# Optimization experiments

Measured on AMD Instinct MI355X. Metric: run time of the kernel, lower is better.

Reference implementation:

```python
import jax, jax.numpy as jnp
import numpy as np

N_NODES = 50000
N_EDGES = 800000
N_GRAPHS = 256
W_SCALE = 0.05  # keep activations bounded through 5 relu conv layers


def setup_inputs() -> dict:
    key = jax.random.key(0)
    ks = jax.random.split(key, 16)
    rn = lambda k, shape: W_SCALE * jax.random.normal(k, shape, dtype=jnp.float32)
    return {
        "x": jax.random.normal(ks[0], (N_NODES, 336), dtype=jnp.float32),
        "edge_index": jax.random.randint(ks[1], (2, N_EDGES), 0, N_NODES, dtype=jnp.int32),
        "batch": jnp.sort(jax.random.randint(ks[2], (N_NODES,), 0, N_GRAPHS, dtype=jnp.int32)),
        "w1_rel": rn(ks[3], (100, 336)),
        "w1_root": rn(ks[4], (100, 336)),
        "b1": rn(ks[5], (100,)),
        "w_rel": rn(ks[6], (4, 100, 100)),
        "w_root": rn(ks[7], (4, 100, 100)),
        "b": rn(ks[8], (4, 100)),
        "lw1": rn(ks[9], (100, 100)),
        "lb1": rn(ks[10], (100,)),
        "lw2": rn(ks[11], (100, 100)),
        "lb2": rn(ks[12], (100,)),
        "lw3": rn(ks[13], (29, 100)),
        "lb3": rn(ks[14], (29,)),
    }


def _graph_conv(x, edge_index, w_rel, w_root, bias):
    # PyG GraphConv: out_i = W_rel @ (sum_{j->i} x_j) + b + W_root @ x_i
    src, dst = edge_index[0], edge_index[1]
    agg = jax.ops.segment_sum(x[src], dst, num_segments=x.shape[0])  # [N, d_in]
    return agg @ w_rel.T + bias + x @ w_root.T


def reference(x, edge_index, batch, w1_rel, w1_root, b1, w_rel, w_root, b,
              lw1, lb1, lw2, lb2, lw3, lb3):
    h = jax.nn.relu(_graph_conv(x, edge_index, w1_rel, w1_root, b1))  # [N,100]
    for i in range(4):  # conv2..conv5 (structurally distinct params)
        h = jax.nn.relu(_graph_conv(h, edge_index, w_rel[i], w_root[i], b[i]))
    # global_mean_pool over graphs
    sums = jax.ops.segment_sum(h, batch, num_segments=N_GRAPHS)          # [G,100]
    counts = jax.ops.segment_sum(jnp.ones((h.shape[0],), h.dtype), batch,
                                 num_segments=N_GRAPHS)                  # [G]
    pooled = sums / jnp.maximum(counts, 1.0)[:, None]
    h = jax.nn.relu(pooled @ lw1.T + lb1)
    h = jax.nn.relu(h @ lw2.T + lb2)
    return h @ lw3.T + lb3  # [G, 29]
```

## Files before the change

### kernel.cpp

```cpp
#include <hip/hip_runtime.h>

#define N_NODES 50000
#define N_EDGES 800000
#define N_GRAPHS 256
#define F 100

#define SCAN_B 512
#define SCAN_NB 98
#define SCAN_PAD (SCAN_NB * SCAN_B)

#define PART_SZ 6250
#define FILL_CHUNK 2048

#define SROW 72
#define EPS 264
#define AST 264

typedef __attribute__((ext_vector_type(8))) short bf16x8;
typedef __attribute__((ext_vector_type(4))) float f32x4;
typedef unsigned short ushort_t;
typedef unsigned int uint_t;

__device__ inline ushort_t f2bf(float f) {
  uint_t u = __float_as_uint(f);
  uint_t r = (u + 0x7fffu + ((u >> 16) & 1u)) >> 16;
  return (ushort_t)r;
}


__global__ __launch_bounds__(256) void hist_kernel(const int* __restrict__ dst,
                                                   int* __restrict__ cnt, int E) {
  int part = blockIdx.x & 7;
  int lo = part * PART_SZ, hi = lo + PART_SZ;
  int base = (blockIdx.x >> 3) * FILL_CHUNK;
  int end = base + FILL_CHUNK; if (end > E) end = E;
  for (int i = base + threadIdx.x; i < end; i += 256) {
    int d = dst[i];
    if (d >= lo && d < hi) atomicAdd(&cnt[d], 1);
  }
}

__global__ __launch_bounds__(SCAN_B) void scan1_kernel(const int* __restrict__ cnt,
                                                       int* __restrict__ excl,
                                                       int* __restrict__ bsum) {
  __shared__ int sh[SCAN_B];
  int t = threadIdx.x;
  int i = blockIdx.x * SCAN_B + t;
  int v = cnt[i];
  sh[t] = v;
  __syncthreads();
  for (int off = 1; off < SCAN_B; off <<= 1) {
    int u = (t >= off) ? sh[t - off] : 0;
    __syncthreads();
    sh[t] += u;
    __syncthreads();
  }
  excl[i] = sh[t] - v;
  if (t == SCAN_B - 1) bsum[blockIdx.x] = sh[t];
}

__global__ __launch_bounds__(128) void scan2_kernel(int* __restrict__ bsum) {
  __shared__ int sh[128];
  int t = threadIdx.x;
  int v = (t < SCAN_NB) ? bsum[t] : 0;
  sh[t] = v;
  __syncthreads();
  for (int off = 1; off < 128; off <<= 1) {
    int u = (t >= off) ? sh[t - off] : 0;
    __syncthreads();
    sh[t] += u;
    __syncthreads();
  }
  if (t < SCAN_NB) bsum[t] = sh[t] - v;
}

__global__ __launch_bounds__(SCAN_B) void scan3_kernel(const int* __restrict__ excl,
                                                       const int* __restrict__ bsum,
                                                       int* __restrict__ offs,
                                                       int* __restrict__ cursor) {
  int i = blockIdx.x * SCAN_B + threadIdx.x;
  int v = excl[i] + bsum[blockIdx.x];
  if (i <= N_NODES) { offs[i] = v; cursor[i] = v; }
}

__global__ __launch_bounds__(256) void fill_kernel(const int* __restrict__ src,
                                                   const int* __restrict__ dst,
                                                   int* __restrict__ cursor,
                                                   int* __restrict__ csr_src, int E) {
  int part = blockIdx.x & 7;
  int lo = part * PART_SZ, hi = lo + PART_SZ;
  int base = (blockIdx.x >> 3) * FILL_CHUNK;
  int end = base + FILL_CHUNK; if (end > E) end = E;
  for (int i = base + threadIdx.x; i < end; i += 256) {
    int d = dst[i];
    if (d >= lo && d < hi) {
      int p = atomicAdd(&cursor[d], 1);
      csr_src[p] = src[i];
    }
  }
}


__global__ void pack_w1_kernel(const float* __restrict__ w1_rel, const float* __restrict__ w1_root,
                               ushort_t* __restrict__ Wp1) {
  int row = blockIdx.x;
  for (int k = threadIdx.x; k < 384; k += 128) {
    float v = 0.f;
    if (k < 336) {
      if (row < 100) v = w1_rel[row * 336 + k];
      else if (row < 200) v = w1_root[(row - 100) * 336 + k];
    }
    Wp1[(size_t)row * 384 + k] = f2bf(v);
  }
}

__global__ void pack_wf_kernel(const float* __restrict__ w_rel, const float* __restrict__ w_root,
                               ushort_t* __restrict__ Wf) {
  int rowl = blockIdx.x;
  int l = rowl >> 7, row = rowl & 127;
  int k = threadIdx.x;
  float v = 0.f;
  if (row < 100) {
    if (k < 100) v = w_rel[((size_t)l * 100 + row) * 100 + k];
    else if (k >= 128 && k < 228) v = w_root[((size_t)l * 100 + row) * 100 + (k - 128)];
  }
  Wf[(size_t)rowl * 256 + k] = f2bf(v);
}


template <bool AF32>
__global__ __launch_bounds__(256) void conv_mfma(
    const void* __restrict__ Aptr, const ushort_t* __restrict__ Wp,
    const float* __restrict__ bias,
    ushort_t* __restrict__ ZP, int Kp) {
  __shared__ short smem[64 * SROW + 208 * SROW];
  __shared__ float bias_s[104];
  short* alds = smem;
  short* blds = smem + 64 * SROW;

  int tid = threadIdx.x;
  int n0 = blockIdx.x * 64;
  if (tid < 100) bias_s[tid] = bias[tid];

  f32x4 acc[13];
#pragma unroll
  for (int b = 0; b < 13; ++b) acc[b] = (f32x4)0.f;

  int w = tid >> 6, lane = tid & 63, q = lane >> 4, m16 = lane & 15;

  int ar[2], aq[2];
#pragma unroll
  for (int u = 0; u < 2; ++u) { int c = tid + u * 256; ar[u] = c >> 3; aq[u] = c & 7; }

  bf16x8 areg[2], breg[7];

  auto load_chunk = [&](int k0) {
#pragma unroll
    for (int u = 0; u < 2; ++u) {
      int node = n0 + ar[u];
      int k = k0 + aq[u] * 8;
      bf16x8 val = (bf16x8)0;
      if (AF32) {
        if (node < N_NODES && k < 336) {
          const float* p = (const float*)Aptr + (size_t)node * 336 + k;
          float4 f0 = *(const float4*)p;
          float4 f1 = *(const float4*)(p + 4);
          val[0] = (short)f2bf(f0.x); val[1] = (short)f2bf(f0.y);
          val[2] = (short)f2bf(f0.z); val[3] = (short)f2bf(f0.w);
          val[4] = (short)f2bf(f1.x); val[5] = (short)f2bf(f1.y);
          val[6] = (short)f2bf(f1.z); val[7] = (short)f2bf(f1.w);
        }
      } else {
        if (node < N_NODES)
          val = *(const bf16x8*)((const short*)Aptr + (size_t)node * 128 + k);
      }
      areg[u] = val;
    }
#pragma unroll
    for (int u = 0; u < 7; ++u) {
      int c = tid + u * 256;
      if (c < 1664) {
        int r = c >> 3, qq = c & 7;
        breg[u] = *(const bf16x8*)((const short*)Wp + (size_t)r * Kp + k0 + qq * 8);
      }
    }
  };

  load_chunk(0);

  for (int k0 = 0; k0 < Kp; k0 += 64) {
#pragma unroll
    for (int u = 0; u < 2; ++u)
      *(bf16x8*)&alds[ar[u] * SROW + aq[u] * 8] = areg[u];
#pragma unroll
    for (int u = 0; u < 7; ++u) {
      int c = tid + u * 256;
      if (c < 1664) {
        int r = c >> 3, qq = c & 7;
        *(bf16x8*)&blds[r * SROW + qq * 8] = breg[u];
      }
    }
    __syncthreads();
    if (k0 + 64 < Kp) load_chunk(k0 + 64);
#pragma unroll
    for (int s = 0; s < 2; ++s) {
      bf16x8 a = *(const bf16x8*)&alds[(w * 16 + m16) * SROW + s * 32 + q * 8];
#pragma unroll
      for (int b = 0; b < 13; ++b) {
        bf16x8 bf = *(const bf16x8*)&blds[(b * 16 + m16) * SROW + s * 32 + q * 8];
        acc[b] = __builtin_amdgcn_mfma_f32_16x16x32_bf16(a, bf, acc[b], 0, 0, 0);
      }
    }
    __syncthreads();
  }

  short* ep = smem;
#pragma unroll
  for (int b = 0; b < 13; ++b) {
    int n = b * 16 + m16;
    if (n < 200) {
      int c = (n < 100) ? n : (n + 28);
      float add = (n < 100) ? 0.f : bias_s[(n - 100) & 127];
#pragma unroll
      for (int r = 0; r < 4; ++r) {
        int row = w * 16 + q * 4 + r;
        ep[row * EPS + c] = (short)f2bf(acc[b][r] + add);
      }
    }
  }
  __syncthreads();
#pragma unroll
  for (int j = 0; j < 8; ++j) {
    int i = tid + j * 256;
    int row = i >> 5, c16 = i & 31;
    int node = n0 + row;
    if (node < N_NODES) {
      *(uint4*)(ZP + (size_t)node * 256 + c16 * 8) =
          *(const uint4*)&ep[row * EPS + c16 * 8];
    }
  }
}


__global__ __launch_bounds__(256) void gather_bf16(
    const ushort_t* __restrict__ ZP,
    const int* __restrict__ offs, const int* __restrict__ csr,
    ushort_t* __restrict__ H) {
  int node = blockIdx.x * 4 + (threadIdx.x >> 6);
  node = __builtin_amdgcn_readfirstlane(node);
  int lane = threadIdx.x & 63;
  int off = (lane < 50 ? lane : 49) * 2;

  uint_t z = *(const uint_t*)(ZP + (size_t)node * 256 + 128 + off);
  float p0[8], p1[8];
#pragma unroll
  for (int u = 0; u < 8; ++u) { p0[u] = 0.f; p1[u] = 0.f; }
  p0[0] = __uint_as_float(z << 16);
  p1[0] = __uint_as_float(z & 0xffff0000u);

  int s = offs[node], e = offs[node + 1];
  for (int j = s; j < e; j += 64) {
    int take = e - j; if (take > 64) take = 64;
    int vidx = (lane < take) ? csr[j + lane] : 0;
    int u = 0;
    for (; u + 8 <= take; u += 8) {
      uint_t zz[8];
#pragma unroll
      for (int t = 0; t < 8; ++t) {
        int idx = __builtin_amdgcn_readlane(vidx, u + t);
        zz[t] = *(const uint_t*)(ZP + (size_t)idx * 256 + off);
      }
#pragma unroll
      for (int t = 0; t < 8; ++t) {
        p0[t] += __uint_as_float(zz[t] << 16);
        p1[t] += __uint_as_float(zz[t] & 0xffff0000u);
      }
    }
    int cnt = take - u;
    if (cnt > 0) {
      uint_t zz[7];
#pragma unroll
      for (int t = 0; t < 7; ++t) {
        if (t < cnt) {
          int idx = __builtin_amdgcn_readlane(vidx, u + t);
          zz[t] = *(const uint_t*)(ZP + (size_t)idx * 256 + off);
        }
      }
#pragma unroll
      for (int t = 0; t < 7; ++t) {
        if (t < cnt) {
          p0[t] += __uint_as_float(zz[t] << 16);
          p1[t] += __uint_as_float(zz[t] & 0xffff0000u);
        }
      }
    }
  }
  float a0 = ((p0[0] + p0[1]) + (p0[2] + p0[3])) + ((p0[4] + p0[5]) + (p0[6] + p0[7]));
  float a1 = ((p1[0] + p1[1]) + (p1[2] + p1[3])) + ((p1[4] + p1[5]) + (p1[6] + p1[7]));
  a0 = fmaxf(a0, 0.f);
  a1 = fmaxf(a1, 0.f);
  uint_t outp = (uint_t)f2bf(a0) | ((uint_t)f2bf(a1) << 16);
  if (lane >= 50) outp = 0u;
  *(uint_t*)(H + (size_t)node * 128 + lane * 2) = outp;
}


__global__ __launch_bounds__(512) void fused_layer(
    const ushort_t* __restrict__ Hin,
    const ushort_t* __restrict__ Wf,
    const float* __restrict__ bias,
    const int* __restrict__ offs, const int* __restrict__ csr,
    ushort_t* __restrict__ Hout) {
  __shared__ short alds[16 * AST];

  int tid = threadIdx.x;
  int w = tid >> 6, lane = tid & 63, q = lane >> 4, m16 = lane & 15;
  int tile = blockIdx.x;

  for (int sub = 0; sub < 2; ++sub) {
    int row = w * 2 + sub;
    int node = tile * 16 + row;
    node = __builtin_amdgcn_readfirstlane(node);
    uint_t hv = *(const uint_t*)(Hin + (size_t)node * 128 + lane * 2);
    *(uint_t*)&alds[row * AST + 128 + lane * 2] = hv;
    int off = (lane < 50 ? lane : 49) * 2;
    float p0[8], p1[8];
#pragma unroll
    for (int u = 0; u < 8; ++u) { p0[u] = 0.f; p1[u] = 0.f; }
    int s = offs[node], e = offs[node + 1];
    for (int j = s; j < e; j += 64) {
      int take = e - j; if (take > 64) take = 64;
      int vidx = (lane < take) ? csr[j + lane] : 0;
      int u = 0;
      for (; u + 8 <= take; u += 8) {
        uint_t zz[8];
#pragma unroll
        for (int t = 0; t < 8; ++t) {
          int idx = __builtin_amdgcn_readlane(vidx, u + t);
          zz[t] = *(const uint_t*)(Hin + (size_t)idx * 128 + off);
        }
#pragma unroll
        for (int t = 0; t < 8; ++t) {
          p0[t] += __uint_as_float(zz[t] << 16);
          p1[t] += __uint_as_float(zz[t] & 0xffff0000u);
        }
      }
      int cnt = take - u;
      if (cnt > 0) {
        uint_t zz[7];
#pragma unroll
        for (int t = 0; t < 7; ++t) {
          if (t < cnt) {
            int idx = __builtin_amdgcn_readlane(vidx, u + t);
            zz[t] = *(const uint_t*)(Hin + (size_t)idx * 128 + off);
          }
        }
#pragma unroll
        for (int t = 0; t < 7; ++t) {
          if (t < cnt) {
            p0[t] += __uint_as_float(zz[t] << 16);
            p1[t] += __uint_as_float(zz[t] & 0xffff0000u);
          }
        }
      }
    }
    float a0 = ((p0[0] + p0[1]) + (p0[2] + p0[3])) + ((p0[4] + p0[5]) + (p0[6] + p0[7]));
    float a1 = ((p1[0] + p1[1]) + (p1[2] + p1[3])) + ((p1[4] + p1[5]) + (p1[6] + p1[7]));
    uint_t outp = (uint_t)f2bf(a0) | ((uint_t)f2bf(a1) << 16);
    if (lane >= 50) outp = 0u;
    *(uint_t*)&alds[row * AST + lane * 2] = outp;
  }

  bf16x8 wreg[8];
#pragma unroll
  for (int s = 0; s < 8; ++s)
    wreg[s] = *(const bf16x8*)(Wf + (size_t)(w * 16 + m16) * 256 + s * 32 + q * 8);
  int n0 = w * 16 + q * 4;
  float4 bb = make_float4(0.f, 0.f, 0.f, 0.f);
  if (n0 < 100) bb = *(const float4*)(bias + n0);

  __syncthreads();

  f32x4 acc = (f32x4)0.f;
#pragma unroll
  for (int s = 0; s < 8; ++s) {
    bf16x8 af = *(const bf16x8*)&alds[m16 * AST + s * 32 + q * 8];
    acc = __builtin_amdgcn_mfma_f32_16x16x32_bf16(wreg[s], af, acc, 0, 0, 0);
  }

  int node = tile * 16 + m16;
  ushort4 v;
  v.x = f2bf(fmaxf(acc[0] + bb.x, 0.f));
  v.y = f2bf(fmaxf(acc[1] + bb.y, 0.f));
  v.z = f2bf(fmaxf(acc[2] + bb.z, 0.f));
  v.w = f2bf(fmaxf(acc[3] + bb.w, 0.f));
  *(ushort4*)(Hout + (size_t)node * 128 + n0) = v;
}


__global__ __launch_bounds__(1024) void pool_kernel(const ushort_t* __restrict__ H,
                                                    const int* __restrict__ batch,
                                                    float* __restrict__ pooled) {
  int g = blockIdx.x;
  int t = threadIdx.x;
  int lo = 0, hi = N_NODES;
  while (lo < hi) { int mid = (lo + hi) >> 1; if (batch[mid] < g) lo = mid + 1; else hi = mid; }
  int s = lo;
  hi = N_NODES;
  while (lo < hi) { int mid = (lo + hi) >> 1; if (batch[mid] <= g) lo = mid + 1; else hi = mid; }
  int e = lo;

  int row = t >> 6;
  int lane = t & 63;
  int off = (lane < 50 ? lane : 49) * 2;
  float a0 = 0.f, a1 = 0.f;
  for (int n = s + row; n < e; n += 16) {
    uint_t z = *(const uint_t*)(H + (size_t)n * 128 + off);
    a0 += __uint_as_float(z << 16);
    a1 += __uint_as_float(z & 0xffff0000u);
  }
  __shared__ float sh[16][104];
  if (lane < 50) { sh[row][lane * 2] = a0; sh[row][lane * 2 + 1] = a1; }
  __syncthreads();
  if (t < 100) {
    float acc = 0.f;
#pragma unroll
    for (int r = 0; r < 16; ++r) acc += sh[r][t];
    int cnt = e - s;
    float d = (cnt > 0) ? (float)cnt : 1.f;
    pooled[(size_t)g * F + t] = acc / d;
  }
}


__global__ void mlp_kernel(const float* __restrict__ pooled,
                           const float* __restrict__ lw1, const float* __restrict__ lb1,
                           const float* __restrict__ lw2, const float* __restrict__ lb2,
                           const float* __restrict__ lw3, const float* __restrict__ lb3,
                           float* __restrict__ out) {
  int g = blockIdx.x;
  int t = threadIdx.x;
  __shared__ float r0[F], r1[F], r2[F];
  if (t < F) r0[t] = pooled[(size_t)g * F + t];
  __syncthreads();
  if (t < F) {
    float s = lb1[t];
    for (int k = 0; k < F; ++k) s += r0[k] * lw1[t * F + k];
    r1[t] = fmaxf(s, 0.f);
  }
  __syncthreads();
  if (t < F) {
    float s = lb2[t];
    for (int k = 0; k < F; ++k) s += r1[k] * lw2[t * F + k];
    r2[t] = fmaxf(s, 0.f);
  }
  __syncthreads();
  if (t < 29) {
    float s = lb3[t];
    for (int k = 0; k < F; ++k) s += r2[k] * lw3[t * F + k];
    out[g * 29 + t] = s;
  }
}


extern "C" void kernel_launch(void* const* d_in, const int* in_sizes, int n_in,
                              void* d_out, int out_size, void* d_ws, size_t ws_size,
                              hipStream_t stream) {
  const float* x       = (const float*)d_in[0];
  const int*   ei      = (const int*)d_in[1];
  const int*   batch   = (const int*)d_in[2];
  const float* w1_rel  = (const float*)d_in[3];
  const float* w1_root = (const float*)d_in[4];
  const float* b1      = (const float*)d_in[5];
  const float* w_rel   = (const float*)d_in[6];
  const float* w_root  = (const float*)d_in[7];
  const float* bvec    = (const float*)d_in[8];
  const float* lw1     = (const float*)d_in[9];
  const float* lb1     = (const float*)d_in[10];
  const float* lw2     = (const float*)d_in[11];
  const float* lb2     = (const float*)d_in[12];
  const float* lw3     = (const float*)d_in[13];
  const float* lb3     = (const float*)d_in[14];
  float* out = (float*)d_out;

  char* ws = (char*)d_ws;
  size_t o = 0;
  auto alloc = [&](size_t bytes) { void* p = ws + o; o = (o + bytes + 511) & ~(size_t)511; return p; };
  ushort_t* H1   = (ushort_t*)alloc((size_t)N_NODES * 128 * 2);
  ushort_t* H2   = (ushort_t*)alloc((size_t)N_NODES * 128 * 2);
  ushort_t* ZP   = (ushort_t*)alloc((size_t)N_NODES * 256 * 2);
  ushort_t* Wp1  = (ushort_t*)alloc((size_t)208 * 384 * 2);
  ushort_t* Wf   = (ushort_t*)alloc((size_t)4 * 128 * 256 * 2);
  float*    pooled = (float*)alloc((size_t)N_GRAPHS * F * 4);
  int* cnt    = (int*)alloc((size_t)SCAN_PAD * 4);
  int* excl   = (int*)alloc((size_t)SCAN_PAD * 4);
  int* bsum   = (int*)alloc((size_t)128 * 4);
  int* offs   = (int*)alloc((size_t)(N_NODES + 1) * 4);
  int* cursor = (int*)alloc((size_t)(N_NODES + 1) * 4);
  int* csr    = (int*)alloc((size_t)N_EDGES * 4);

  const int E = N_EDGES;
  const int* srcv = ei;
  const int* dstv = ei + E;

  int nchunk = (E + FILL_CHUNK - 1) / FILL_CHUNK;
  hipMemsetAsync(cnt, 0, (size_t)SCAN_PAD * sizeof(int), stream);
  hist_kernel<<<nchunk * 8, 256, 0, stream>>>(dstv, cnt, E);
  scan1_kernel<<<SCAN_NB, SCAN_B, 0, stream>>>(cnt, excl, bsum);
  scan2_kernel<<<1, 128, 0, stream>>>(bsum);
  scan3_kernel<<<SCAN_NB, SCAN_B, 0, stream>>>(excl, bsum, offs, cursor);
  fill_kernel<<<nchunk * 8, 256, 0, stream>>>(srcv, dstv, cursor, csr, E);

  pack_w1_kernel<<<208, 128, 0, stream>>>(w1_rel, w1_root, Wp1);
  pack_wf_kernel<<<512, 256, 0, stream>>>(w_rel, w_root, Wf);

  int mmgrid = (N_NODES + 63) / 64;
  conv_mfma<true><<<mmgrid, 256, 0, stream>>>(x, Wp1, b1, ZP, 384);
  gather_bf16<<<N_NODES / 4, 256, 0, stream>>>(ZP, offs, csr, H1);

  const ushort_t* hin = H1;
  ushort_t* hout = H2;
  for (int l = 0; l < 4; ++l) {
    fused_layer<<<N_NODES / 16, 512, 0, stream>>>(hin, Wf + (size_t)l * 128 * 256,
                                                  bvec + (size_t)l * F, offs, csr, hout);
    const ushort_t* tmp = hout; hout = (ushort_t*)hin; hin = tmp;
  }
  pool_kernel<<<N_GRAPHS, 1024, 0, stream>>>(hin, batch, pooled);
  mlp_kernel<<<N_GRAPHS, 128, 0, stream>>>(pooled, lw1, lb1, lw2, lb2, lw3, lb3, out);
}
```

Before: 457.0 us.

## Pad CSR to sentinel-filled multiples of eight and merge small kernels

Each node's CSR segment is padded up to a multiple of 8 and filled with a sentinel index that points at a zeroed extra row in ZP/H1/H2. The gather loops can then drop their tail handling and run a double-buffered 8-wide load/consume pipeline. The three scan kernels become one single-block scan, the weight packing, memset and sentinel init are folded into one pack_all kernel, and pool and MLP are fused. Weight and bias loads in fused_layer are hoisted ahead of the gather. The cost is roughly 40% more gathered edges from padding and a serial single-block scan.

```diff
diff --git a/kernel.cpp b/kernel.cpp
--- a/kernel.cpp
+++ b/kernel.cpp
@@ -5,16 +5,18 @@
 #define N_GRAPHS 256
 #define F 100
 
-#define SCAN_B 512
-#define SCAN_NB 98
-#define SCAN_PAD (SCAN_NB * SCAN_B)
+#define SCAN_PAD 50176
 
 #define PART_SZ 6250
 #define FILL_CHUNK 2048
+#define HIST_BLOCKS 3128
 
 #define SROW 72
 #define EPS 264
 #define AST 264
+
+#define SENT N_NODES
+#define CSR_CAP 1155072
 
 typedef __attribute__((ext_vector_type(8))) short bf16x8;
 typedef __attribute__((ext_vector_type(4))) float f32x4;
@@ -25,6 +27,51 @@
   uint_t u = __float_as_uint(f);
   uint_t r = (u + 0x7fffu + ((u >> 16) & 1u)) >> 16;
   return (ushort_t)r;
+}
+
+
+__global__ __launch_bounds__(256) void pack_all(
+    const float* __restrict__ w1_rel, const float* __restrict__ w1_root,
+    const float* __restrict__ w_rel, const float* __restrict__ w_root,
+    ushort_t* __restrict__ Wp1, ushort_t* __restrict__ Wf, int* __restrict__ cnt,
+    int* __restrict__ csr, ushort_t* __restrict__ ZP,
+    ushort_t* __restrict__ H1, ushort_t* __restrict__ H2) {
+  int b = blockIdx.x;
+  int tid = threadIdx.x;
+  if (b < 208) {
+    int row = b;
+    for (int k = tid; k < 384; k += 256) {
+      float v = 0.f;
+      if (k < 336) {
+        if (row < 100) v = w1_rel[row * 336 + k];
+        else if (row < 200) v = w1_root[(row - 100) * 336 + k];
+      }
+      Wp1[(size_t)row * 384 + k] = f2bf(v);
+    }
+  } else if (b < 720) {
+    int rowl = b - 208;
+    int l = rowl >> 7, row = rowl & 127;
+    int k = tid;
+    float v = 0.f;
+    if (row < 100) {
+      if (k < 100) v = w_rel[((size_t)l * 100 + row) * 100 + k];
+      else if (k >= 128 && k < 228) v = w_root[((size_t)l * 100 + row) * 100 + (k - 128)];
+    }
+    Wf[(size_t)rowl * 256 + k] = f2bf(v);
+  } else if (b < 769) {
+    int z = b - 720;
+    *(int4*)(cnt + (size_t)z * 1024 + tid * 4) = make_int4(0, 0, 0, 0);
+  } else if (b < 1051) {
+    int i0 = (b - 769) * 4096 + tid * 16;
+    int4 sv = make_int4(SENT, SENT, SENT, SENT);
+    *(int4*)(csr + i0) = sv; *(int4*)(csr + i0 + 4) = sv;
+    *(int4*)(csr + i0 + 8) = sv; *(int4*)(csr + i0 + 12) = sv;
+  } else {
+    uint4 z4 = make_uint4(0u, 0u, 0u, 0u);
+    if (tid < 32)      *(uint4*)(ZP + (size_t)SENT * 256 + tid * 8) = z4;
+    else if (tid < 48) *(uint4*)(H1 + (size_t)SENT * 128 + (tid - 32) * 8) = z4;
+    else if (tid < 64) *(uint4*)(H2 + (size_t)SENT * 128 + (tid - 48) * 8) = z4;
+  }
 }
 
 
@@ -40,48 +87,32 @@
   }
 }
 
-__global__ __launch_bounds__(SCAN_B) void scan1_kernel(const int* __restrict__ cnt,
-                                                       int* __restrict__ excl,
-                                                       int* __restrict__ bsum) {
-  __shared__ int sh[SCAN_B];
+
+__global__ __launch_bounds__(1024) void scan_all(const int* __restrict__ cnt,
+                                                 int* __restrict__ offs,
+                                                 int* __restrict__ cursor) {
+  __shared__ int part[1024];
   int t = threadIdx.x;
-  int i = blockIdx.x * SCAN_B + t;
-  int v = cnt[i];
-  sh[t] = v;
-  __syncthreads();
-  for (int off = 1; off < SCAN_B; off <<= 1) {
-    int u = (t >= off) ? sh[t - off] : 0;
+  int base = t * 49;
+  int s = 0;
+  for (int i = 0; i < 49; ++i) s += (cnt[base + i] + 7) & ~7;
+  part[t] = s;
+  __syncthreads();
+  for (int off = 1; off < 1024; off <<= 1) {
+    int u = (t >= off) ? part[t - off] : 0;
     __syncthreads();
-    sh[t] += u;
+    part[t] += u;
     __syncthreads();
   }
-  excl[i] = sh[t] - v;
-  if (t == SCAN_B - 1) bsum[blockIdx.x] = sh[t];
-}
-
-__global__ __launch_bounds__(128) void scan2_kernel(int* __restrict__ bsum) {
-  __shared__ int sh[128];
-  int t = threadIdx.x;
-  int v = (t < SCAN_NB) ? bsum[t] : 0;
-  sh[t] = v;
-  __syncthreads();
-  for (int off = 1; off < 128; off <<= 1) {
-    int u = (t >= off) ? sh[t - off] : 0;
-    __syncthreads();
-    sh[t] += u;
-    __syncthreads();
-  }
-  if (t < SCAN_NB) bsum[t] = sh[t] - v;
-}
-
-__global__ __launch_bounds__(SCAN_B) void scan3_kernel(const int* __restrict__ excl,
-                                                       const int* __restrict__ bsum,
-                                                       int* __restrict__ offs,
-                                                       int* __restrict__ cursor) {
-  int i = blockIdx.x * SCAN_B + threadIdx.x;
-  int v = excl[i] + bsum[blockIdx.x];
-  if (i <= N_NODES) { offs[i] = v; cursor[i] = v; }
-}
+  int run = part[t] - s;
+  for (int i = 0; i < 49; ++i) {
+    int idx = base + i;
+    int slot = (cnt[idx] + 7) & ~7;
+    if (idx <= N_NODES) { offs[idx] = run; cursor[idx] = run; }
+    run += slot;
+  }
+}
+
 
 __global__ __launch_bounds__(256) void fill_kernel(const int* __restrict__ src,
                                                    const int* __restrict__ dst,
@@ -98,33 +129,6 @@
       csr_src[p] = src[i];
     }
   }
-}
-
-
-__global__ void pack_w1_kernel(const float* __restrict__ w1_rel, const float* __restrict__ w1_root,
-                               ushort_t* __restrict__ Wp1) {
-  int row = blockIdx.x;
-  for (int k = threadIdx.x; k < 384; k += 128) {
-    float v = 0.f;
-    if (k < 336) {
-      if (row < 100) v = w1_rel[row * 336 + k];
-      else if (row < 200) v = w1_root[(row - 100) * 336 + k];
-    }
-    Wp1[(size_t)row * 384 + k] = f2bf(v);
-  }
-}
-
-__global__ void pack_wf_kernel(const float* __restrict__ w_rel, const float* __restrict__ w_root,
-                               ushort_t* __restrict__ Wf) {
-  int rowl = blockIdx.x;
-  int l = rowl >> 7, row = rowl & 127;
-  int k = threadIdx.x;
-  float v = 0.f;
-  if (row < 100) {
-    if (k < 100) v = w_rel[((size_t)l * 100 + row) * 100 + k];
-    else if (k >= 128 && k < 228) v = w_root[((size_t)l * 100 + row) * 100 + (k - 128)];
-  }
-  Wf[(size_t)rowl * 256 + k] = f2bf(v);
 }
 
 
@@ -246,10 +250,10 @@
     const ushort_t* __restrict__ ZP,
     const int* __restrict__ offs, const int* __restrict__ csr,
     ushort_t* __restrict__ H) {
+  int lane = threadIdx.x & 63;
+  int off = (lane < 50 ? lane : 49) * 2;
   int node = blockIdx.x * 4 + (threadIdx.x >> 6);
   node = __builtin_amdgcn_readfirstlane(node);
-  int lane = threadIdx.x & 63;
-  int off = (lane < 50 ? lane : 49) * 2;
 
   uint_t z = *(const uint_t*)(ZP + (size_t)node * 256 + 128 + off);
   float p0[8], p1[8];
@@ -259,41 +263,48 @@
   p1[0] = __uint_as_float(z & 0xffff0000u);
 
   int s = offs[node], e = offs[node + 1];
+  uint_t zA[8], zB[8];
   for (int j = s; j < e; j += 64) {
-    int take = e - j; if (take > 64) take = 64;
-    int vidx = (lane < take) ? csr[j + lane] : 0;
-    int u = 0;
-    for (; u + 8 <= take; u += 8) {
-      uint_t zz[8];
+    int rem = e - j;
+    int ng = (rem > 64 ? 64 : rem) >> 3;
+    int vidx = csr[j + lane];
+    auto loadA = [&](int g) {
 #pragma unroll
       for (int t = 0; t < 8; ++t) {
-        int idx = __builtin_amdgcn_readlane(vidx, u + t);
-        zz[t] = *(const uint_t*)(ZP + (size_t)idx * 256 + off);
-      }
+        int idx = __builtin_amdgcn_readlane(vidx, g * 8 + t);
+        zA[t] = *(const uint_t*)(ZP + (size_t)idx * 256 + off);
+      }
+    };
+    auto loadB = [&](int g) {
 #pragma unroll
       for (int t = 0; t < 8; ++t) {
-        p0[t] += __uint_as_float(zz[t] << 16);
-        p1[t] += __uint_as_float(zz[t] & 0xffff0000u);
-      }
-    }
-    int cnt = take - u;
-    if (cnt > 0) {
-      uint_t zz[7];
-#pragma unroll
-      for (int t = 0; t < 7; ++t) {
-        if (t < cnt) {
-          int idx = __builtin_amdgcn_readlane(vidx, u + t);
-          zz[t] = *(const uint_t*)(ZP + (size_t)idx * 256 + off);
-        }
-      }
-#pragma unroll
-      for (int t = 0; t < 7; ++t) {
-        if (t < cnt) {
-          p0[t] += __uint_as_float(zz[t] << 16);
-          p1[t] += __uint_as_float(zz[t] & 0xffff0000u);
-        }
-      }
-    }
+        int idx = __builtin_amdgcn_readlane(vidx, g * 8 + t);
+        zB[t] = *(const uint_t*)(ZP + (size_t)idx * 256 + off);
+      }
+    };
+    auto consA = [&]() {
+#pragma unroll
+      for (int t = 0; t < 8; ++t) {
+        p0[t] += __uint_as_float(zA[t] << 16);
+        p1[t] += __uint_as_float(zA[t] & 0xffff0000u);
+      }
+    };
+    auto consB = [&]() {
+#pragma unroll
+      for (int t = 0; t < 8; ++t) {
+        p0[t] += __uint_as_float(zB[t] << 16);
+        p1[t] += __uint_as_float(zB[t] & 0xffff0000u);
+      }
+    };
+    loadA(0);
+    int g = 0;
+    for (; g + 2 <= ng; g += 2) {
+      loadB(g + 1);
+      consA();
+      if (g + 2 < ng) loadA(g + 2);
+      consB();
+    }
+    if (g < ng) consA();
   }
   float a0 = ((p0[0] + p0[1]) + (p0[2] + p0[3])) + ((p0[4] + p0[5]) + (p0[6] + p0[7]));
   float a1 = ((p1[0] + p1[1]) + (p1[2] + p1[3])) + ((p1[4] + p1[5]) + (p1[6] + p1[7]));
@@ -317,52 +328,67 @@
   int w = tid >> 6, lane = tid & 63, q = lane >> 4, m16 = lane & 15;
   int tile = blockIdx.x;
 
+  bf16x8 wreg[8];
+#pragma unroll
+  for (int s = 0; s < 8; ++s)
+    wreg[s] = *(const bf16x8*)(Wf + (size_t)(w * 16 + m16) * 256 + s * 32 + q * 8);
+  int n0 = w * 16 + q * 4;
+  float4 bb = make_float4(0.f, 0.f, 0.f, 0.f);
+  if (n0 < 100) bb = *(const float4*)(bias + n0);
+
+  int off = (lane < 50 ? lane : 49) * 2;
   for (int sub = 0; sub < 2; ++sub) {
     int row = w * 2 + sub;
     int node = tile * 16 + row;
     node = __builtin_amdgcn_readfirstlane(node);
     uint_t hv = *(const uint_t*)(Hin + (size_t)node * 128 + lane * 2);
     *(uint_t*)&alds[row * AST + 128 + lane * 2] = hv;
-    int off = (lane < 50 ? lane : 49) * 2;
     float p0[8], p1[8];
 #pragma unroll
     for (int u = 0; u < 8; ++u) { p0[u] = 0.f; p1[u] = 0.f; }
     int s = offs[node], e = offs[node + 1];
+    uint_t zA[8], zB[8];
     for (int j = s; j < e; j += 64) {
-      int take = e - j; if (take > 64) take = 64;
-      int vidx = (lane < take) ? csr[j + lane] : 0;
-      int u = 0;
-      for (; u + 8 <= take; u += 8) {
-        uint_t zz[8];
+      int rem = e - j;
+      int ng = (rem > 64 ? 64 : rem) >> 3;
+      int vidx = csr[j + lane];
+      auto loadA = [&](int g) {
 #pragma unroll
         for (int t = 0; t < 8; ++t) {
-          int idx = __builtin_amdgcn_readlane(vidx, u + t);
-          zz[t] = *(const uint_t*)(Hin + (size_t)idx * 128 + off);
+          int idx = __builtin_amdgcn_readlane(vidx, g * 8 + t);
+          zA[t] = *(const uint_t*)(Hin + (size_t)idx * 128 + off);
         }
+      };
+      auto loadB = [&](int g) {
 #pragma unroll
         for (int t = 0; t < 8; ++t) {
-          p0[t] += __uint_as_float(zz[t] << 16);
-          p1[t] += __uint_as_float(zz[t] & 0xffff0000u);
+          int idx = __builtin_amdgcn_readlane(vidx, g * 8 + t);
+          zB[t] = *(const uint_t*)(Hin + (size_t)idx * 128 + off);
         }
-      }
-      int cnt = take - u;
-      if (cnt > 0) {
-        uint_t zz[7];
-#pragma unroll
-        for (int t = 0; t < 7; ++t) {
-          if (t < cnt) {
-            int idx = __builtin_amdgcn_readlane(vidx, u + t);
-            zz[t] = *(const uint_t*)(Hin + (size_t)idx * 128 + off);
-          }
+      };
+      auto consA = [&]() {
+#pragma unroll
+        for (int t = 0; t < 8; ++t) {
+          p0[t] += __uint_as_float(zA[t] << 16);
+          p1[t] += __uint_as_float(zA[t] & 0xffff0000u);
         }
-#pragma unroll
-        for (int t = 0; t < 7; ++t) {
-          if (t < cnt) {
-            p0[t] += __uint_as_float(zz[t] << 16);
-            p1[t] += __uint_as_float(zz[t] & 0xffff0000u);
-          }
+      };
+      auto consB = [&]() {
+#pragma unroll
+        for (int t = 0; t < 8; ++t) {
+          p0[t] += __uint_as_float(zB[t] << 16);
+          p1[t] += __uint_as_float(zB[t] & 0xffff0000u);
         }
-      }
+      };
+      loadA(0);
+      int g = 0;
+      for (; g + 2 <= ng; g += 2) {
+        loadB(g + 1);
+        consA();
+        if (g + 2 < ng) loadA(g + 2);
+        consB();
+      }
+      if (g < ng) consA();
     }
     float a0 = ((p0[0] + p0[1]) + (p0[2] + p0[3])) + ((p0[4] + p0[5]) + (p0[6] + p0[7]));
     float a1 = ((p1[0] + p1[1]) + (p1[2] + p1[3])) + ((p1[4] + p1[5]) + (p1[6] + p1[7]));
@@ -370,37 +396,29 @@
     if (lane >= 50) outp = 0u;
     *(uint_t*)&alds[row * AST + lane * 2] = outp;
   }
-
-  bf16x8 wreg[8];
-#pragma unroll
-  for (int s = 0; s < 8; ++s)
-    wreg[s] = *(const bf16x8*)(Wf + (size_t)(w * 16 + m16) * 256 + s * 32 + q * 8);
-  int n0 = w * 16 + q * 4;
-  float4 bb = make_float4(0.f, 0.f, 0.f, 0.f);
-  if (n0 < 100) bb = *(const float4*)(bias + n0);
-
-  __syncthreads();
-
+  __syncthreads();
   f32x4 acc = (f32x4)0.f;
 #pragma unroll
   for (int s = 0; s < 8; ++s) {
     bf16x8 af = *(const bf16x8*)&alds[m16 * AST + s * 32 + q * 8];
     acc = __builtin_amdgcn_mfma_f32_16x16x32_bf16(wreg[s], af, acc, 0, 0, 0);
   }
-
-  int node = tile * 16 + m16;
+  int nodeo = tile * 16 + m16;
   ushort4 v;
   v.x = f2bf(fmaxf(acc[0] + bb.x, 0.f));
   v.y = f2bf(fmaxf(acc[1] + bb.y, 0.f));
   v.z = f2bf(fmaxf(acc[2] + bb.z, 0.f));
   v.w = f2bf(fmaxf(acc[3] + bb.w, 0.f));
-  *(ushort4*)(Hout + (size_t)node * 128 + n0) = v;
-}
-
-
-__global__ __launch_bounds__(1024) void pool_kernel(const ushort_t* __restrict__ H,
-                                                    const int* __restrict__ batch,
-                                                    float* __restrict__ pooled) {
+  *(ushort4*)(Hout + (size_t)nodeo * 128 + n0) = v;
+}
+
+
+__global__ __launch_bounds__(1024) void pool_mlp(
+    const ushort_t* __restrict__ H, const int* __restrict__ batch,
+    const float* __restrict__ lw1, const float* __restrict__ lb1,
+    const float* __restrict__ lw2, const float* __restrict__ lb2,
+    const float* __restrict__ lw3, const float* __restrict__ lb3,
+    float* __restrict__ out) {
   int g = blockIdx.x;
   int t = threadIdx.x;
   int lo = 0, hi = N_NODES;
@@ -420,45 +438,34 @@
     a1 += __uint_as_float(z & 0xffff0000u);
   }
   __shared__ float sh[16][104];
+  __shared__ float r0[F], r1[F], r2[F];
   if (lane < 50) { sh[row][lane * 2] = a0; sh[row][lane * 2 + 1] = a1; }
   __syncthreads();
-  if (t < 100) {
+  if (t < F) {
     float acc = 0.f;
 #pragma unroll
     for (int r = 0; r < 16; ++r) acc += sh[r][t];
     int cnt = e - s;
     float d = (cnt > 0) ? (float)cnt : 1.f;
-    pooled[(size_t)g * F + t] = acc / d;
-  }
-}
-
-
-__global__ void mlp_kernel(const float* __restrict__ pooled,
-                           const float* __restrict__ lw1, const float* __restrict__ lb1,
-                           const float* __restrict__ lw2, const float* __restrict__ lb2,
-                           const float* __restrict__ lw3, const float* __restrict__ lb3,
-                           float* __restrict__ out) {
-  int g = blockIdx.x;
-  int t = threadIdx.x;
-  __shared__ float r0[F], r1[F], r2[F];
-  if (t < F) r0[t] = pooled[(size_t)g * F + t];
+    r0[t] = acc / d;
+  }
   __syncthreads();
   if (t < F) {
-    float s = lb1[t];
-    for (int k = 0; k < F; ++k) s += r0[k] * lw1[t * F + k];
-    r1[t] = fmaxf(s, 0.f);
+    float sv = lb1[t];
+    for (int k = 0; k < F; ++k) sv += r0[k] * lw1[t * F + k];
+    r1[t] = fmaxf(sv, 0.f);
   }
   __syncthreads();
   if (t < F) {
-    float s = lb2[t];
-    for (int k = 0; k < F; ++k) s += r1[k] * lw2[t * F + k];
-    r2[t] = fmaxf(s, 0.f);
+    float sv = lb2[t];
+    for (int k = 0; k < F; ++k) sv += r1[k] * lw2[t * F + k];
+    r2[t] = fmaxf(sv, 0.f);
   }
   __syncthreads();
   if (t < 29) {
-    float s = lb3[t];
-    for (int k = 0; k < F; ++k) s += r2[k] * lw3[t * F + k];
-    out[g * 29 + t] = s;
+    float sv = lb3[t];
+    for (int k = 0; k < F; ++k) sv += r2[k] * lw3[t * F + k];
+    out[g * 29 + t] = sv;
   }
 }
 
@@ -486,33 +493,24 @@
   char* ws = (char*)d_ws;
   size_t o = 0;
   auto alloc = [&](size_t bytes) { void* p = ws + o; o = (o + bytes + 511) & ~(size_t)511; return p; };
-  ushort_t* H1   = (ushort_t*)alloc((size_t)N_NODES * 128 * 2);
-  ushort_t* H2   = (ushort_t*)alloc((size_t)N_NODES * 128 * 2);
-  ushort_t* ZP   = (ushort_t*)alloc((size_t)N_NODES * 256 * 2);
+  ushort_t* H1   = (ushort_t*)alloc((size_t)(N_NODES + 1) * 128 * 2);
+  ushort_t* H2   = (ushort_t*)alloc((size_t)(N_NODES + 1) * 128 * 2);
+  ushort_t* ZP   = (ushort_t*)alloc((size_t)(N_NODES + 1) * 256 * 2);
   ushort_t* Wp1  = (ushort_t*)alloc((size_t)208 * 384 * 2);
   ushort_t* Wf   = (ushort_t*)alloc((size_t)4 * 128 * 256 * 2);
-  float*    pooled = (float*)alloc((size_t)N_GRAPHS * F * 4);
   int* cnt    = (int*)alloc((size_t)SCAN_PAD * 4);
-  int* excl   = (int*)alloc((size_t)SCAN_PAD * 4);
-  int* bsum   = (int*)alloc((size_t)128 * 4);
   int* offs   = (int*)alloc((size_t)(N_NODES + 1) * 4);
   int* cursor = (int*)alloc((size_t)(N_NODES + 1) * 4);
-  int* csr    = (int*)alloc((size_t)N_EDGES * 4);
+  int* csr    = (int*)alloc((size_t)CSR_CAP * 4);
 
   const int E = N_EDGES;
   const int* srcv = ei;
   const int* dstv = ei + E;
 
-  int nchunk = (E + FILL_CHUNK - 1) / FILL_CHUNK;
-  hipMemsetAsync(cnt, 0, (size_t)SCAN_PAD * sizeof(int), stream);
-  hist_kernel<<<nchunk * 8, 256, 0, stream>>>(dstv, cnt, E);
-  scan1_kernel<<<SCAN_NB, SCAN_B, 0, stream>>>(cnt, excl, bsum);
-  scan2_kernel<<<1, 128, 0, stream>>>(bsum);
-  scan3_kernel<<<SCAN_NB, SCAN_B, 0, stream>>>(excl, bsum, offs, cursor);
-  fill_kernel<<<nchunk * 8, 256, 0, stream>>>(srcv, dstv, cursor, csr, E);
-
-  pack_w1_kernel<<<208, 128, 0, stream>>>(w1_rel, w1_root, Wp1);
-  pack_wf_kernel<<<512, 256, 0, stream>>>(w_rel, w_root, Wf);
+  pack_all<<<1052, 256, 0, stream>>>(w1_rel, w1_root, w_rel, w_root, Wp1, Wf, cnt, csr, ZP, H1, H2);
+  hist_kernel<<<HIST_BLOCKS, 256, 0, stream>>>(dstv, cnt, E);
+  scan_all<<<1, 1024, 0, stream>>>(cnt, offs, cursor);
+  fill_kernel<<<HIST_BLOCKS, 256, 0, stream>>>(srcv, dstv, cursor, csr, E);
 
   int mmgrid = (N_NODES + 63) / 64;
   conv_mfma<true><<<mmgrid, 256, 0, stream>>>(x, Wp1, b1, ZP, 384);
@@ -525,6 +523,5 @@
                                                   bvec + (size_t)l * F, offs, csr, hout);
     const ushort_t* tmp = hout; hout = (ushort_t*)hin; hin = tmp;
   }
-  pool_kernel<<<N_GRAPHS, 1024, 0, stream>>>(hin, batch, pooled);
-  mlp_kernel<<<N_GRAPHS, 128, 0, stream>>>(pooled, lw1, lb1, lw2, lb2, lw3, lb3, out);
-}
+  pool_mlp<<<N_GRAPHS, 1024, 0, stream>>>(hin, batch, lw1, lb1, lw2, lb2, lw3, lb3, out);
+}
```

Result: slower. 576.1 us (+26.1%).
